# Kernel optimization log

Measured on AMD Instinct MI355X. Metric: run time of the kernel, lower is better.

## Reference

```python
import jax, jax.numpy as jnp
import numpy as np

NF, NA, NC = 100000, 400, 30   # flight, airport, carrier node counts
N = NF + NA + NC               # total nodes after type concatenation
D = 256                        # hidden_channels
B = 3                          # num_bases
R = 4                          # num_relations
E = 250000                     # edges per relation


def setup_inputs() -> dict:
    key = jax.random.key(0)
    ks = jax.random.split(key, 32)
    inp = {
        'x_flight': jax.random.normal(ks[0], (NF, 32), jnp.float32),
        'x_airport': jax.random.normal(ks[1], (NA, 16), jnp.float32),
        'x_carrier': jax.random.normal(ks[2], (NC, 8), jnp.float32),
        # per-type encoders (Linear stored as [in, out])
        'W_f': jax.random.normal(ks[3], (32, D), jnp.float32) * 0.05,
        'b_f': jnp.zeros((D,), jnp.float32),
        'W_a': jax.random.normal(ks[4], (16, D), jnp.float32) * 0.05,
        'b_a': jnp.zeros((D,), jnp.float32),
        'W_c': jax.random.normal(ks[5], (8, D), jnp.float32) * 0.05,
        'b_c': jnp.zeros((D,), jnp.float32),
        # RGCNConv layer 0: basis decomposition W_r = sum_b comp[r,b] * basis[b]
        'basis0': jax.random.normal(ks[6], (B, D, D), jnp.float32) * 0.02,
        'comp0': jax.random.normal(ks[7], (R, B), jnp.float32) * 0.5,
        'root0': jax.random.normal(ks[8], (D, D), jnp.float32) * 0.02,
        'bias0': jnp.zeros((D,), jnp.float32),
        # RGCNConv layer 1
        'basis1': jax.random.normal(ks[9], (B, D, D), jnp.float32) * 0.02,
        'comp1': jax.random.normal(ks[10], (R, B), jnp.float32) * 0.5,
        'root1': jax.random.normal(ks[11], (D, D), jnp.float32) * 0.02,
        'bias1': jnp.zeros((D,), jnp.float32),
        # readout Linear(D -> 1)
        'W_out': jax.random.normal(ks[12], (D, 1), jnp.float32) * 0.05,
        'b_out': jnp.zeros((1,), jnp.float32),
        # per-relation edge lists (local indices within src/dst node type)
        'src0': jax.random.randint(ks[13], (E,), 0, NF),
        'dst0': jax.random.randint(ks[14], (E,), 0, NA),
        'src1': jax.random.randint(ks[15], (E,), 0, NA),
        'dst1': jax.random.randint(ks[16], (E,), 0, NF),
        'src2': jax.random.randint(ks[17], (E,), 0, NF),
        'dst2': jax.random.randint(ks[18], (E,), 0, NC),
        'src3': jax.random.randint(ks[19], (E,), 0, NC),
        'dst3': jax.random.randint(ks[20], (E,), 0, NF),
    }
    return inp


def _rgcn_conv(x, basis, comp, root, bias, edges):
    """PyG RGCNConv with basis decomposition, mean aggregation per relation."""
    W = jnp.einsum('rb,bio->rio', comp, basis)  # [R, D, D]
    out = x @ root + bias                        # root/self transform
    for r, (src, dst) in enumerate(edges):       # R=4 fixed relations
        msg = x[src] @ W[r]                                        # [E, D]
        agg = jax.ops.segment_sum(msg, dst, num_segments=N)        # [N, D]
        deg = jax.ops.segment_sum(jnp.ones((dst.shape[0],), x.dtype), dst,
                                  num_segments=N)
        out = out + agg / jnp.maximum(deg, 1.0)[:, None]           # mean aggr
    return out


def reference(x_flight, x_airport, x_carrier,
              W_f, b_f, W_a, b_a, W_c, b_c,
              basis0, comp0, root0, bias0,
              basis1, comp1, root1, bias1,
              W_out, b_out,
              src0, dst0, src1, dst1, src2, dst2, src3, dst3):
    # per-type encoders + ReLU, then concat into homogeneous node tensor
    hf = jax.nn.relu(x_flight @ W_f + b_f)
    ha = jax.nn.relu(x_airport @ W_a + b_a)
    hc = jax.nn.relu(x_carrier @ W_c + b_c)
    x = jnp.concatenate([hf, ha, hc], axis=0)  # offsets: flight=0, airport=NF, carrier=NF+NA
    edges = [
        (src0, dst0 + NF),        # flight -> airport
        (src1 + NF, dst1),        # airport -> flight
        (src2, dst2 + NF + NA),   # flight -> carrier
        (src3 + NF + NA, dst3),   # carrier -> flight
    ]
    x = jax.nn.relu(_rgcn_conv(x, basis0, comp0, root0, bias0, edges))
    x = jax.nn.relu(_rgcn_conv(x, basis1, comp1, root1, bias1, edges))
    # dropout is identity in eval mode
    return (x[:NF] @ W_out + b_out).squeeze(-1)  # [NF]
```

## Files before the change

### kernel.cpp

```cpp
#include <hip/hip_runtime.h>
#include <hip/hip_bf16.h>
#include <cstdint>
#include <cstddef>

constexpr int NF = 100000;
constexpr int NA = 400;
constexpr int NC = 30;
constexpr int NN = NF + NA + NC;
constexpr int D  = 256;
constexpr int DD = D * D;
constexpr int E  = 250000;
constexpr int NSL = 128;

typedef __attribute__((ext_vector_type(8))) short bf16x8;
typedef __attribute__((ext_vector_type(4))) float f32x4;
typedef __attribute__((ext_vector_type(8))) ushort u16x8;

__device__ inline ushort f2bf(float f) {
    __hip_bfloat16 h = __float2bfloat16(f);
    return __builtin_bit_cast(ushort, h);
}
__device__ inline float bf2f(ushort u) {
    __hip_bfloat16 h = __builtin_bit_cast(__hip_bfloat16, u);
    return __bfloat162float(h);
}

__device__ inline void gload_lds16(const ushort* g, ushort* l) {
    __builtin_amdgcn_global_load_lds(
        (const __attribute__((address_space(1))) void*)g,
        (__attribute__((address_space(3))) void*)l, 16, 0, 0);
}

template<int K, int ROWS>
__global__ __launch_bounds__(256) void encode_kernel(
    const float* __restrict__ x, const float* __restrict__ W,
    const float* __restrict__ b, ushort* __restrict__ hH,
    int rows, int row_off)
{
    int c = threadIdx.x;
    int base = blockIdx.x * ROWS;
    float wcol[K];
    #pragma unroll
    for (int k = 0; k < K; ++k) wcol[k] = W[k * D + c];
    float bias = b[c];
    for (int i = 0; i < ROWS; ++i) {
        int row = base + i;
        if (row >= rows) return;
        const float* xr = x + (size_t)row * K;
        float acc = bias;
        #pragma unroll
        for (int k = 0; k < K; ++k) acc += xr[k] * wcol[k];
        hH[(size_t)(row_off + row) * D + c] = f2bf(fmaxf(acc, 0.f));
    }
}

__global__ __launch_bounds__(256) void wsplit_kernel(
    const float* __restrict__ root, ushort* __restrict__ WtH, ushort* __restrict__ WtL)
{
    int n = blockIdx.x, k = threadIdx.x;
    float w = root[(size_t)k * D + n];
    ushort hi = f2bf(w);
    WtH[(size_t)n * D + k] = hi;
    WtL[(size_t)n * D + k] = f2bf(w - bf2f(hi));
}

__global__ __launch_bounds__(256) void wr_kernel(
    const float* __restrict__ basis, const float* __restrict__ comp,
    float* __restrict__ wr)
{
    int idx = blockIdx.x * 256 + threadIdx.x;
    int r = idx >> 16;
    int io = idx & (DD - 1);
    wr[idx] = comp[r * 3 + 0] * basis[io]
            + comp[r * 3 + 1] * basis[DD + io]
            + comp[r * 3 + 2] * basis[2 * DD + io];
}

__global__ __launch_bounds__(256) void deg_count_kernel(
    const int* __restrict__ dst1, const int* __restrict__ dst3,
    int* __restrict__ deg1, int* __restrict__ deg3)
{
    int idx = blockIdx.x * 256 + threadIdx.x;
    if (idx >= 2 * E) return;
    if (idx < E) atomicAdd(&deg1[dst1[idx]], 1);
    else         atomicAdd(&deg3[dst3[idx - E]], 1);
}

__global__ __launch_bounds__(256) void hist02_kernel(
    const int* __restrict__ dst0, const int* __restrict__ dst2,
    int* __restrict__ bh0, int* __restrict__ bh2)
{
    __shared__ int hist[NA];
    int b = blockIdx.x;
    bool isR2 = (b >= NSL);
    int sl = isR2 ? b - NSL : b;
    const int* dst = isR2 ? dst2 : dst0;
    int nb = isR2 ? NC : NA;
    for (int i = threadIdx.x; i < nb; i += 256) hist[i] = 0;
    __syncthreads();
    int lo = (int)((long long)E * sl / NSL);
    int hi = (int)((long long)E * (sl + 1) / NSL);
    for (int e = lo + threadIdx.x; e < hi; e += 256)
        atomicAdd(&hist[dst[e]], 1);
    __syncthreads();
    int* bh = isR2 ? (bh2 + sl * NC) : (bh0 + sl * NA);
    for (int i = threadIdx.x; i < nb; i += 256) bh[i] = hist[i];
}

__global__ __launch_bounds__(512) void scan02_kernel(
    int* __restrict__ bh0, int* __restrict__ bh2,
    int* __restrict__ rp0, int* __restrict__ rp2,
    float* __restrict__ inv0, float* __restrict__ inv2)
{
    __shared__ int tot[512];
    __shared__ int exc[512];
    int t = threadIdx.x;
    int cnt = 0;
    if (t < NA) {
        int s = 0;
        for (int sl = 0; sl < NSL; ++sl) {
            int v = bh0[sl * NA + t]; bh0[sl * NA + t] = s; s += v;
        }
        cnt = s;
    } else if (t < NA + NC) {
        int bin = t - NA; int s = 0;
        for (int sl = 0; sl < NSL; ++sl) {
            int v = bh2[sl * NC + bin]; bh2[sl * NC + bin] = s; s += v;
        }
        cnt = s;
    }
    tot[t] = cnt;
    __syncthreads();
    for (int ofs = 1; ofs < 512; ofs <<= 1) {
        int v = (t >= ofs) ? tot[t - ofs] : 0;
        __syncthreads();
        tot[t] += v;
        __syncthreads();
    }
    int ex = tot[t] - cnt;
    if (t < NA) {
        exc[t] = ex;
        rp0[t] = ex;
        inv0[t] = 1.0f / (float)(cnt > 1 ? cnt : 1);
        if (t == 0) { rp0[NA] = E; rp2[NC] = E; }
    } else if (t < NA + NC) {
        exc[t] = ex - E;
        rp2[t - NA] = ex - E;
        inv2[t - NA] = 1.0f / (float)(cnt > 1 ? cnt : 1);
    } else exc[t] = 0;
    __syncthreads();
    for (int idx = t; idx < NSL * NA; idx += 512) {
        int sl = idx / NA; int bin = idx - sl * NA;
        bh0[idx] += exc[bin];
    }
    for (int idx = t; idx < NSL * NC; idx += 512) {
        int sl = idx / NC; int bin = idx - sl * NC;
        bh2[idx] += exc[NA + bin];
    }
}

__global__ __launch_bounds__(256) void fill02_kernel(
    const int* __restrict__ src0, const int* __restrict__ dst0,
    const int* __restrict__ src2, const int* __restrict__ dst2,
    const int* __restrict__ bh0, const int* __restrict__ bh2,
    int* __restrict__ csr0, int* __restrict__ csr2)
{
    __shared__ int cur[NA];
    int b = blockIdx.x;
    bool isR2 = (b >= NSL);
    int sl = isR2 ? b - NSL : b;
    const int* src = isR2 ? src2 : src0;
    const int* dst = isR2 ? dst2 : dst0;
    const int* bh  = isR2 ? (bh2 + sl * NC) : (bh0 + sl * NA);
    int* csr       = isR2 ? csr2 : csr0;
    int nb = isR2 ? NC : NA;
    for (int i = threadIdx.x; i < nb; i += 256) cur[i] = bh[i];
    __syncthreads();
    int lo = (int)((long long)E * sl / NSL);
    int hi = (int)((long long)E * (sl + 1) / NSL);
    for (int e = lo + threadIdx.x; e < hi; e += 256) {
        int pos = atomicAdd(&cur[dst[e]], 1);
        csr[pos] = src[e];
    }
}

__global__ __launch_bounds__(1024) void scanA_kernel(
    const int* __restrict__ deg1, const int* __restrict__ deg3, int* __restrict__ bsum)
{
    __shared__ int s[1024];
    int b = blockIdx.x;
    bool isR3 = (b >= 98);
    const int* deg = isR3 ? deg3 : deg1;
    int chunk = isR3 ? b - 98 : b;
    int i = chunk * 1024 + threadIdx.x;
    int v = (i < NF) ? deg[i] : 0;
    s[threadIdx.x] = v;
    __syncthreads();
    for (int ofs = 512; ofs > 0; ofs >>= 1) {
        if ((int)threadIdx.x < ofs) s[threadIdx.x] += s[threadIdx.x + ofs];
        __syncthreads();
    }
    if (threadIdx.x == 0) bsum[(isR3 ? 128 : 0) + chunk] = s[0];
}

__global__ __launch_bounds__(256) void scanB_kernel(int* __restrict__ bsum)
{
    __shared__ int s[256];
    int t = threadIdx.x;
    int v = ((t & 127) < 98) ? bsum[t] : 0;
    s[t] = v;
    __syncthreads();
    for (int ofs = 1; ofs < 128; ofs <<= 1) {
        int a = ((t & 127) >= ofs) ? s[t - ofs] : 0;
        __syncthreads();
        s[t] += a;
        __syncthreads();
    }
    bsum[t] = s[t] - v;
}

__global__ __launch_bounds__(1024) void scanC_kernel(
    const int* __restrict__ deg1, const int* __restrict__ deg3,
    const int* __restrict__ bsum,
    int* __restrict__ rp1, int* __restrict__ rp3,
    int* __restrict__ cu1, int* __restrict__ cu3,
    float* __restrict__ inv1, float* __restrict__ inv3)
{
    __shared__ int s[1024];
    int b = blockIdx.x;
    const int* deg; int* rp; int* cu; float* inv; int chunk; int prefix;
    if (b < 98) { deg = deg1; rp = rp1; cu = cu1; inv = inv1; chunk = b;      prefix = bsum[chunk]; }
    else        { deg = deg3; rp = rp3; cu = cu3; inv = inv3; chunk = b - 98; prefix = bsum[128 + chunk]; }
    int tid = threadIdx.x;
    int i = chunk * 1024 + tid;
    int v = (i < NF) ? deg[i] : 0;
    s[tid] = v;
    __syncthreads();
    for (int ofs = 1; ofs < 1024; ofs <<= 1) {
        int a = (tid >= ofs) ? s[tid - ofs] : 0;
        __syncthreads();
        s[tid] += a;
        __syncthreads();
    }
    int ex = prefix + s[tid] - v;
    if (i < NF) {
        rp[i] = ex;
        cu[i] = ex;
        inv[i] = 1.0f / (float)(v > 1 ? v : 1);
    }
    if (i == 0) rp[NF] = E;
}

__global__ __launch_bounds__(256) void csr_fill13_kernel(
    const int* __restrict__ src1, const int* __restrict__ dst1,
    const int* __restrict__ src3, const int* __restrict__ dst3,
    int* __restrict__ cu1, int* __restrict__ cu3,
    int* __restrict__ csr1, int* __restrict__ csr3)
{
    int idx = blockIdx.x * 256 + threadIdx.x;
    if (idx >= 2 * E) return;
    if (idx < E) {
        int pos = atomicAdd(&cu1[dst1[idx]], 1);
        csr1[pos] = src1[idx];
    } else {
        int e = idx - E;
        int pos = atomicAdd(&cu3[dst3[e]], 1);
        csr3[pos] = src3[e];
    }
}

__global__ __launch_bounds__(256) void y_kernel(
    const ushort* __restrict__ hH, const float* __restrict__ wr,
    float* __restrict__ y)
{
    int row = blockIdx.x;
    int c = threadIdx.x;
    const ushort* sH = hH + (size_t)(NF + row) * D;
    const float* W = wr + (size_t)((row < NA) ? 1 : 3) * DD;
    float acc = 0.f;
    #pragma unroll 8
    for (int k = 0; k < D; ++k) acc += bf2f(sH[k]) * W[k * D + c];
    y[(size_t)row * D + c] = acc;
}

__global__ __launch_bounds__(512) void gemm_mfma(
    const ushort* __restrict__ A,
    const ushort* __restrict__ WtH, const ushort* __restrict__ WtL,
    const float* __restrict__ bias,
    ushort* __restrict__ G, int nrows)
{
    constexpr int BM = 128, BK = 32;
    constexpr int PLANE = BM * BK;
    constexpr int BUF = 3 * PLANE;
    constexpr int LDW = 36;
    __shared__ __align__(16) ushort lds[2 * BUF];
    const int t = threadIdx.x;
    const int row0 = blockIdx.x * BM;
    const int col0 = blockIdx.y * BM;
    const int w = t >> 6, lane = t & 63;
    const int wm = w >> 2, wn = w & 3;
    const int lr = lane & 15;
    const int lk = lane >> 4;
    f32x4 acc[4][2] = {};

    const ushort* sp[3];
    int dofs[3];
    #pragma unroll
    for (int i = 0; i < 3; ++i) {
        int idx = w * 3 + i;
        int plane = idx >> 3, g = idx & 7;
        const ushort* base = (plane == 0) ? A : (plane == 1) ? WtH : WtL;
        int r = ((plane == 0) ? row0 : col0) + g * 16 + lr;
        if (plane == 0 && r >= nrows) r = nrows - 1;
        sp[i] = base + (size_t)r * D + lk * 8;
        dofs[i] = plane * PLANE + g * 512;
    }

    auto stage = [&](int k0, int buf) {
        ushort* bb = lds + buf * BUF;
        #pragma unroll
        for (int i = 0; i < 3; ++i)
            gload_lds16(sp[i] + k0, bb + dofs[i]);
    };
    auto compute = [&](int buf) {
        const ushort* base = lds + buf * BUF;
        const ushort* As  = base;
        const ushort* WsH = base + PLANE;
        const ushort* WsL = base + 2 * PLANE;
        bf16x8 bh[2], bl[2];
        #pragma unroll
        for (int ni = 0; ni < 2; ++ni) {
            int off = (wn * 2 + ni) * 512 + lane * 8;
            bh[ni] = *(const bf16x8*)(&WsH[off]);
            bl[ni] = *(const bf16x8*)(&WsL[off]);
        }
        #pragma unroll
        for (int mi = 0; mi < 4; ++mi) {
            int off = (wm * 4 + mi) * 512 + lane * 8;
            bf16x8 ah = *(const bf16x8*)(&As[off]);
            #pragma unroll
            for (int ni = 0; ni < 2; ++ni) {
                acc[mi][ni] = __builtin_amdgcn_mfma_f32_16x16x32_bf16(ah, bh[ni], acc[mi][ni], 0, 0, 0);
                acc[mi][ni] = __builtin_amdgcn_mfma_f32_16x16x32_bf16(ah, bl[ni], acc[mi][ni], 0, 0, 0);
            }
        }
    };

    stage(0, 0);
    asm volatile("s_waitcnt vmcnt(0)" ::: "memory");
    __builtin_amdgcn_s_barrier();
    __builtin_amdgcn_sched_barrier(0);
    for (int kt = 0; kt < 7; ++kt) {
        stage((kt + 1) * BK, (kt + 1) & 1);
        __builtin_amdgcn_sched_barrier(0);
        compute(kt & 1);
        asm volatile("s_waitcnt vmcnt(0)" ::: "memory");
        __builtin_amdgcn_s_barrier();
        __builtin_amdgcn_sched_barrier(0);
    }
    compute(1);

    __syncthreads();
    float* S = (float*)lds + (size_t)w * 16 * LDW;
    const int rrow = lane >> 2;
    const int grp  = lane & 3;
    #pragma unroll
    for (int mi = 0; mi < 4; ++mi) {
        __syncthreads();
        #pragma unroll
        for (int ni = 0; ni < 2; ++ni)
            #pragma unroll
            for (int reg = 0; reg < 4; ++reg)
                S[(lk * 4 + reg) * LDW + ni * 16 + lr] = acc[mi][ni][reg];
        __syncthreads();
        int gr = row0 + wm * 64 + mi * 16 + rrow;
        int gc = col0 + wn * 32 + grp * 8;
        if (gr >= nrows) continue;
        float4 f0 = *(const float4*)(&S[rrow * LDW + grp * 8]);
        float4 f1 = *(const float4*)(&S[rrow * LDW + grp * 8 + 4]);
        float4 b0 = *(const float4*)(bias + gc);
        float4 b1 = *(const float4*)(bias + gc + 4);
        float v[8] = {f0.x + b0.x, f0.y + b0.y, f0.z + b0.z, f0.w + b0.w,
                      f1.x + b1.x, f1.y + b1.y, f1.z + b1.z, f1.w + b1.w};
        u16x8 hh;
        #pragma unroll
        for (int j = 0; j < 8; ++j) hh[j] = f2bf(v[j]);
        *(u16x8*)(G + (size_t)gr * D + gc) = hh;
    }
}

__global__ __launch_bounds__(256) void msg_relu_kernel(
    ushort* __restrict__ G,
    const float* __restrict__ y,
    const int* __restrict__ rp1, const int* __restrict__ csr1, const float* __restrict__ inv1,
    const int* __restrict__ rp3, const int* __restrict__ csr3, const float* __restrict__ inv3)
{
    int wid = (blockIdx.x * 256 + threadIdx.x) >> 6;
    int lane = threadIdx.x & 63;
    int row = wid * 2 + (lane >> 5);
    if (row >= NF) return;
    int c = (lane & 31) * 8;
    size_t o = (size_t)row * D + c;
    u16x8 gh = *(const u16x8*)(G + o);
    float v[8];
    #pragma unroll
    for (int j = 0; j < 8; ++j) v[j] = bf2f(gh[j]);
    float m[8] = {};
    int e0 = rp1[row], e1 = rp1[row + 1];
    for (int e = e0; e < e1; ++e) {
        const float* yr = y + (size_t)csr1[e] * D + c;
        float4 u0 = *(const float4*)yr;
        float4 u1 = *(const float4*)(yr + 4);
        m[0] += u0.x; m[1] += u0.y; m[2] += u0.z; m[3] += u0.w;
        m[4] += u1.x; m[5] += u1.y; m[6] += u1.z; m[7] += u1.w;
    }
    float s1 = inv1[row];
    #pragma unroll
    for (int j = 0; j < 8; ++j) { v[j] += s1 * m[j]; m[j] = 0.f; }
    e0 = rp3[row]; e1 = rp3[row + 1];
    for (int e = e0; e < e1; ++e) {
        const float* yr = y + (size_t)(NA + csr3[e]) * D + c;
        float4 u0 = *(const float4*)yr;
        float4 u1 = *(const float4*)(yr + 4);
        m[0] += u0.x; m[1] += u0.y; m[2] += u0.z; m[3] += u0.w;
        m[4] += u1.x; m[5] += u1.y; m[6] += u1.z; m[7] += u1.w;
    }
    float s3 = inv3[row];
    u16x8 oh;
    #pragma unroll
    for (int j = 0; j < 8; ++j) oh[j] = f2bf(fmaxf(v[j] + s3 * m[j], 0.f));
    *(u16x8*)(G + o) = oh;
}

__global__ __launch_bounds__(256) void msg_readout_kernel(
    const ushort* __restrict__ G,
    const float* __restrict__ y,
    const int* __restrict__ rp1, const int* __restrict__ csr1, const float* __restrict__ inv1,
    const int* __restrict__ rp3, const int* __restrict__ csr3, const float* __restrict__ inv3,
    const float* __restrict__ wout, const float* __restrict__ bout,
    float* __restrict__ out)
{
    int wid = (blockIdx.x * 256 + threadIdx.x) >> 6;
    int lane = threadIdx.x & 63;
    int row = wid * 2 + (lane >> 5);
    if (row >= NF) return;
    int c = (lane & 31) * 8;
    size_t o = (size_t)row * D + c;
    u16x8 gh = *(const u16x8*)(G + o);
    float v[8];
    #pragma unroll
    for (int j = 0; j < 8; ++j) v[j] = bf2f(gh[j]);
    float m[8] = {};
    int e0 = rp1[row], e1 = rp1[row + 1];
    for (int e = e0; e < e1; ++e) {
        const float* yr = y + (size_t)csr1[e] * D + c;
        float4 u0 = *(const float4*)yr;
        float4 u1 = *(const float4*)(yr + 4);
        m[0] += u0.x; m[1] += u0.y; m[2] += u0.z; m[3] += u0.w;
        m[4] += u1.x; m[5] += u1.y; m[6] += u1.z; m[7] += u1.w;
    }
    float s1 = inv1[row];
    #pragma unroll
    for (int j = 0; j < 8; ++j) { v[j] += s1 * m[j]; m[j] = 0.f; }
    e0 = rp3[row]; e1 = rp3[row + 1];
    for (int e = e0; e < e1; ++e) {
        const float* yr = y + (size_t)(NA + csr3[e]) * D + c;
        float4 u0 = *(const float4*)yr;
        float4 u1 = *(const float4*)(yr + 4);
        m[0] += u0.x; m[1] += u0.y; m[2] += u0.z; m[3] += u0.w;
        m[4] += u1.x; m[5] += u1.y; m[6] += u1.z; m[7] += u1.w;
    }
    float s3 = inv3[row];
    float4 w0 = *(const float4*)(wout + c);
    float4 w1 = *(const float4*)(wout + c + 4);
    float wv[8] = {w0.x, w0.y, w0.z, w0.w, w1.x, w1.y, w1.z, w1.w};
    float pr = 0.f;
    #pragma unroll
    for (int j = 0; j < 8; ++j) pr += fmaxf(v[j] + s3 * m[j], 0.f) * wv[j];
    pr += __shfl_xor(pr, 1);
    pr += __shfl_xor(pr, 2);
    pr += __shfl_xor(pr, 4);
    pr += __shfl_xor(pr, 8);
    pr += __shfl_xor(pr, 16);
    if ((lane & 31) == 0) out[row] = pr + bout[0];
}

__global__ __launch_bounds__(256) void agg_small_kernel(
    const ushort* __restrict__ hH,
    const int* __restrict__ rp0, const int* __restrict__ csr0,
    const int* __restrict__ rp2, const int* __restrict__ csr2,
    float* __restrict__ agg)
{
    __shared__ float red[4][256];
    int b = blockIdx.x;
    const int* rp; const int* csr; int dstn, chunk, nch; float* arow;
    if (b < NA * 4) { dstn = b >> 2; chunk = b & 3; nch = 4;  rp = rp0; csr = csr0; arow = agg + (size_t)dstn * D; }
    else { int bb = b - NA * 4; dstn = bb >> 6; chunk = bb & 63; nch = 64; rp = rp2; csr = csr2; arow = agg + (size_t)(NA + dstn) * D; }
    int s = rp[dstn], e = rp[dstn + 1];
    int cnt = e - s;
    int lo = s + (int)((long long)cnt * chunk / nch);
    int hi = s + (int)((long long)cnt * (chunk + 1) / nch);
    int w = threadIdx.x >> 6, lane = threadIdx.x & 63;
    int span = hi - lo;
    int wlo = lo + (int)((long long)span * w / 4);
    int whi = lo + (int)((long long)span * (w + 1) / 4);
    int half = lane >> 5;
    int ch8 = (lane & 31) * 8;
    float acc[8] = {};
    int p = wlo;
    for (; p + 1 < whi; p += 2) {
        int r = csr[p + half];
        u16x8 v = *(const u16x8*)(hH + (size_t)r * D + ch8);
        #pragma unroll
        for (int j = 0; j < 8; ++j) acc[j] += bf2f(v[j]);
    }
    if (p < whi && half == 0) {
        int r = csr[p];
        u16x8 v = *(const u16x8*)(hH + (size_t)r * D + ch8);
        #pragma unroll
        for (int j = 0; j < 8; ++j) acc[j] += bf2f(v[j]);
    }
    #pragma unroll
    for (int j = 0; j < 8; ++j) acc[j] += __shfl_xor(acc[j], 32);
    if (lane < 32) {
        #pragma unroll
        for (int j = 0; j < 8; ++j) red[w][ch8 + j] = acc[j];
    }
    __syncthreads();
    int c = threadIdx.x;
    float total = red[0][c] + red[1][c] + red[2][c] + red[3][c];
    atomicAdd(arow + c, total);
}

__global__ __launch_bounds__(256) void smallT_kernel(
    const float* __restrict__ agg, const float* __restrict__ wr,
    const float* __restrict__ inv0, const float* __restrict__ inv2,
    ushort* __restrict__ G)
{
    int row = blockIdx.x;
    int c = threadIdx.x;
    const float* a = agg + (size_t)row * D;
    const float* W = wr + (size_t)((row < NA) ? 0 : 2) * DD;
    float scale = (row < NA) ? inv0[row] : inv2[row - NA];
    float acc = 0.f;
    #pragma unroll 8
    for (int k = 0; k < D; ++k) acc += a[k] * W[k * D + c];
    size_t o = (size_t)(NF + row) * D + c;
    G[o] = f2bf(fmaxf(bf2f(G[o]) + scale * acc, 0.f));
}

extern "C" void kernel_launch(void* const* d_in, const int* in_sizes, int n_in,
                              void* d_out, int out_size, void* d_ws, size_t ws_size,
                              hipStream_t stream)
{
    const float* xf = (const float*)d_in[0];
    const float* xa = (const float*)d_in[1];
    const float* xc = (const float*)d_in[2];
    const float* Wf = (const float*)d_in[3];
    const float* bf = (const float*)d_in[4];
    const float* Wa = (const float*)d_in[5];
    const float* ba = (const float*)d_in[6];
    const float* Wc = (const float*)d_in[7];
    const float* bc = (const float*)d_in[8];
    const float* basis0 = (const float*)d_in[9];
    const float* comp0  = (const float*)d_in[10];
    const float* root0  = (const float*)d_in[11];
    const float* bias0  = (const float*)d_in[12];
    const float* basis1 = (const float*)d_in[13];
    const float* comp1  = (const float*)d_in[14];
    const float* root1  = (const float*)d_in[15];
    const float* bias1  = (const float*)d_in[16];
    const float* Wout = (const float*)d_in[17];
    const float* bout = (const float*)d_in[18];
    const int* src0 = (const int*)d_in[19];
    const int* dst0 = (const int*)d_in[20];
    const int* src1 = (const int*)d_in[21];
    const int* dst1 = (const int*)d_in[22];
    const int* src2 = (const int*)d_in[23];
    const int* dst2 = (const int*)d_in[24];
    const int* src3 = (const int*)d_in[25];
    const int* dst3 = (const int*)d_in[26];
    float* out = (float*)d_out;

    char* ws = (char*)d_ws;
    size_t off = 0;
    auto alloc = [&](size_t bytes) -> char* {
        char* p = ws + off;
        off = (off + bytes + 255) & ~(size_t)255;
        return p;
    };
    ushort* hH  = (ushort*)alloc((size_t)NN * D * 2);
    ushort* gH  = (ushort*)alloc((size_t)NN * D * 2);
    ushort* g2H = hH;
    ushort* WtH = (ushort*)alloc((size_t)DD * 2);
    ushort* WtL = (ushort*)alloc((size_t)DD * 2);
    float* wrbuf  = (float*)alloc((size_t)4 * DD * 4);
    float* ybuf   = (float*)alloc((size_t)(NA + NC) * D * 4);
    float* aggbuf = (float*)alloc((size_t)(NA + NC) * D * 4);
    int*   deg13  = (int*)  alloc((size_t)2 * NF * 4);
    int* deg1 = deg13; int* deg3 = deg13 + NF;
    float* inv1 = (float*)alloc((size_t)NF * 4);
    float* inv3 = (float*)alloc((size_t)NF * 4);
    float* inv0 = (float*)alloc((size_t)NA * 4);
    float* inv2 = (float*)alloc((size_t)NC * 4);
    int* rp0 = (int*)alloc((NA + 1) * 4);
    int* rp1 = (int*)alloc((size_t)(NF + 1) * 4);
    int* rp2 = (int*)alloc((NC + 1) * 4);
    int* rp3 = (int*)alloc((size_t)(NF + 1) * 4);
    int* cu1 = (int*)alloc((size_t)(NF + 1) * 4);
    int* cu3 = (int*)alloc((size_t)(NF + 1) * 4);
    int* csr0 = (int*)alloc((size_t)E * 4);
    int* csr1 = (int*)alloc((size_t)E * 4);
    int* csr2 = (int*)alloc((size_t)E * 4);
    int* csr3 = (int*)alloc((size_t)E * 4);
    int* bsum = (int*)alloc(256 * 4);
    int* bh0  = (int*)alloc((size_t)NSL * NA * 4);
    int* bh2  = (int*)alloc((size_t)NSL * NC * 4);
    (void)ws_size; (void)in_sizes; (void)n_in; (void)out_size;

    hist02_kernel<<<2 * NSL, 256, 0, stream>>>(dst0, dst2, bh0, bh2);
    scan02_kernel<<<1, 512, 0, stream>>>(bh0, bh2, rp0, rp2, inv0, inv2);
    fill02_kernel<<<2 * NSL, 256, 0, stream>>>(src0, dst0, src2, dst2, bh0, bh2, csr0, csr2);

    hipMemsetAsync(deg13, 0, (size_t)2 * NF * 4, stream);
    deg_count_kernel<<<(2 * E + 255) / 256, 256, 0, stream>>>(dst1, dst3, deg1, deg3);
    scanA_kernel<<<196, 1024, 0, stream>>>(deg1, deg3, bsum);
    scanB_kernel<<<1, 256, 0, stream>>>(bsum);
    scanC_kernel<<<196, 1024, 0, stream>>>(deg1, deg3, bsum, rp1, rp3, cu1, cu3, inv1, inv3);
    csr_fill13_kernel<<<(2 * E + 255) / 256, 256, 0, stream>>>(
        src1, dst1, src3, dst3, cu1, cu3, csr1, csr3);

    encode_kernel<32, 8><<<NF / 8, 256, 0, stream>>>(xf, Wf, bf, hH, NF, 0);
    encode_kernel<16, 8><<<(NA + 7) / 8, 256, 0, stream>>>(xa, Wa, ba, hH, NA, NF);
    encode_kernel<8, 8><<<(NC + 7) / 8, 256, 0, stream>>>(xc, Wc, bc, hH, NC, NF + NA);

    wsplit_kernel<<<D, D, 0, stream>>>(root0, WtH, WtL);
    wr_kernel<<<4 * DD / 256, 256, 0, stream>>>(basis0, comp0, wrbuf);
    y_kernel<<<NA + NC, 256, 0, stream>>>(hH, wrbuf, ybuf);
    gemm_mfma<<<dim3((NN + 127) / 128, 2), 512, 0, stream>>>(
        hH, WtH, WtL, bias0, gH, NN);
    hipMemsetAsync(aggbuf, 0, (size_t)(NA + NC) * D * 4, stream);
    agg_small_kernel<<<NA * 4 + NC * 64, 256, 0, stream>>>(
        hH, rp0, csr0, rp2, csr2, aggbuf);
    smallT_kernel<<<NA + NC, 256, 0, stream>>>(aggbuf, wrbuf, inv0, inv2, gH);
    msg_relu_kernel<<<(NF / 2 * 64 + 255) / 256, 256, 0, stream>>>(
        gH, ybuf, rp1, csr1, inv1, rp3, csr3, inv3);

    wsplit_kernel<<<D, D, 0, stream>>>(root1, WtH, WtL);
    wr_kernel<<<4 * DD / 256, 256, 0, stream>>>(basis1, comp1, wrbuf);
    y_kernel<<<NA + NC, 256, 0, stream>>>(gH, wrbuf, ybuf);
    gemm_mfma<<<dim3((NF + 127) / 128, 2), 512, 0, stream>>>(
        gH, WtH, WtL, bias1, g2H, NF);
    msg_readout_kernel<<<(NF / 2 * 64 + 255) / 256, 256, 0, stream>>>(
        g2H, ybuf, rp1, csr1, inv1, rp3, csr3, inv3, Wout, bout, out);
}
```

Baseline: 402.9 us.

## Triple-buffer GEMM K-loop and widen per-lane columns in message kernels

The MFMA GEMM moves from a double-buffered to a triple-buffered LDS pipeline. It keeps two tiles of global-to-LDS loads in flight and waits on partial vmcnt counts instead of draining all loads every step. Separately, the message-passing and readout kernels now handle 16 columns per lane and 4 rows per wavefront instead of 8 columns and 2 rows, so each thread issues more independent loads per gathered edge. This adds LDS footprint, which may lower GEMM occupancy, and raises register pressure in the gather kernels.

```diff
diff --git a/kernel.cpp b/kernel.cpp
--- a/kernel.cpp
+++ b/kernel.cpp
@@ -293,7 +293,7 @@
     constexpr int PLANE = BM * BK;
     constexpr int BUF = 3 * PLANE;
     constexpr int LDW = 36;
-    __shared__ __align__(16) ushort lds[2 * BUF];
+    __shared__ __align__(16) ushort lds[3 * BUF];
     const int t = threadIdx.x;
     const int row0 = blockIdx.x * BM;
     const int col0 = blockIdx.y * BM;
@@ -316,8 +316,9 @@
         dofs[i] = plane * PLANE + g * 512;
     }
 
-    auto stage = [&](int k0, int buf) {
+    auto stage = [&](int kt, int buf) {
         ushort* bb = lds + buf * BUF;
+        int k0 = kt * BK;
         #pragma unroll
         for (int i = 0; i < 3; ++i)
             gload_lds16(sp[i] + k0, bb + dofs[i]);
@@ -347,18 +348,25 @@
     };
 
     stage(0, 0);
-    asm volatile("s_waitcnt vmcnt(0)" ::: "memory");
-    __builtin_amdgcn_s_barrier();
-    __builtin_amdgcn_sched_barrier(0);
-    for (int kt = 0; kt < 7; ++kt) {
-        stage((kt + 1) * BK, (kt + 1) & 1);
-        __builtin_amdgcn_sched_barrier(0);
-        compute(kt & 1);
-        asm volatile("s_waitcnt vmcnt(0)" ::: "memory");
-        __builtin_amdgcn_s_barrier();
-        __builtin_amdgcn_sched_barrier(0);
-    }
-    compute(1);
+    stage(1, 1);
+    stage(2, 2);
+#define PIPE_ITER(KT, PEND)                                        \
+    asm volatile("s_waitcnt vmcnt(" #PEND ")" ::: "memory");       \
+    __builtin_amdgcn_s_barrier();                                  \
+    __builtin_amdgcn_sched_barrier(0);                             \
+    compute((KT) % 3);                                             \
+    __builtin_amdgcn_s_barrier();                                  \
+    __builtin_amdgcn_sched_barrier(0);                             \
+    if ((KT) + 3 < 8) stage((KT) + 3, (KT) % 3);
+    PIPE_ITER(0, 6)
+    PIPE_ITER(1, 6)
+    PIPE_ITER(2, 6)
+    PIPE_ITER(3, 6)
+    PIPE_ITER(4, 6)
+    PIPE_ITER(5, 6)
+    PIPE_ITER(6, 3)
+    PIPE_ITER(7, 0)
+#undef PIPE_ITER
 
     __syncthreads();
     float* S = (float*)lds + (size_t)w * 16 * LDW;
@@ -397,39 +405,48 @@
 {
     int wid = (blockIdx.x * 256 + threadIdx.x) >> 6;
     int lane = threadIdx.x & 63;
-    int row = wid * 2 + (lane >> 5);
+    int row = wid * 4 + (lane >> 4);
     if (row >= NF) return;
-    int c = (lane & 31) * 8;
+    int c = (lane & 15) * 16;
     size_t o = (size_t)row * D + c;
-    u16x8 gh = *(const u16x8*)(G + o);
-    float v[8];
-    #pragma unroll
-    for (int j = 0; j < 8; ++j) v[j] = bf2f(gh[j]);
-    float m[8] = {};
+    u16x8 g0 = *(const u16x8*)(G + o);
+    u16x8 g1 = *(const u16x8*)(G + o + 8);
+    float v[16];
+    #pragma unroll
+    for (int j = 0; j < 8; ++j) { v[j] = bf2f(g0[j]); v[8 + j] = bf2f(g1[j]); }
+    float m[16] = {};
     int e0 = rp1[row], e1 = rp1[row + 1];
     for (int e = e0; e < e1; ++e) {
         const float* yr = y + (size_t)csr1[e] * D + c;
-        float4 u0 = *(const float4*)yr;
-        float4 u1 = *(const float4*)(yr + 4);
-        m[0] += u0.x; m[1] += u0.y; m[2] += u0.z; m[3] += u0.w;
-        m[4] += u1.x; m[5] += u1.y; m[6] += u1.z; m[7] += u1.w;
+        #pragma unroll
+        for (int q = 0; q < 4; ++q) {
+            float4 u = *(const float4*)(yr + q * 4);
+            m[q * 4 + 0] += u.x; m[q * 4 + 1] += u.y;
+            m[q * 4 + 2] += u.z; m[q * 4 + 3] += u.w;
+        }
     }
     float s1 = inv1[row];
     #pragma unroll
-    for (int j = 0; j < 8; ++j) { v[j] += s1 * m[j]; m[j] = 0.f; }
+    for (int j = 0; j < 16; ++j) { v[j] += s1 * m[j]; m[j] = 0.f; }
     e0 = rp3[row]; e1 = rp3[row + 1];
     for (int e = e0; e < e1; ++e) {
         const float* yr = y + (size_t)(NA + csr3[e]) * D + c;
-        float4 u0 = *(const float4*)yr;
-        float4 u1 = *(const float4*)(yr + 4);
-        m[0] += u0.x; m[1] += u0.y; m[2] += u0.z; m[3] += u0.w;
-        m[4] += u1.x; m[5] += u1.y; m[6] += u1.z; m[7] += u1.w;
+        #pragma unroll
+        for (int q = 0; q < 4; ++q) {
+            float4 u = *(const float4*)(yr + q * 4);
+            m[q * 4 + 0] += u.x; m[q * 4 + 1] += u.y;
+            m[q * 4 + 2] += u.z; m[q * 4 + 3] += u.w;
+        }
     }
     float s3 = inv3[row];
-    u16x8 oh;
-    #pragma unroll
-    for (int j = 0; j < 8; ++j) oh[j] = f2bf(fmaxf(v[j] + s3 * m[j], 0.f));
-    *(u16x8*)(G + o) = oh;
+    u16x8 o0, o1;
+    #pragma unroll
+    for (int j = 0; j < 8; ++j) {
+        o0[j] = f2bf(fmaxf(v[j] + s3 * m[j], 0.f));
+        o1[j] = f2bf(fmaxf(v[8 + j] + s3 * m[8 + j], 0.f));
+    }
+    *(u16x8*)(G + o) = o0;
+    *(u16x8*)(G + o + 8) = o1;
 }
 
 __global__ __launch_bounds__(256) void msg_readout_kernel(
@@ -442,47 +459,54 @@
 {
     int wid = (blockIdx.x * 256 + threadIdx.x) >> 6;
     int lane = threadIdx.x & 63;
-    int row = wid * 2 + (lane >> 5);
+    int row = wid * 4 + (lane >> 4);
     if (row >= NF) return;
-    int c = (lane & 31) * 8;
+    int c = (lane & 15) * 16;
     size_t o = (size_t)row * D + c;
-    u16x8 gh = *(const u16x8*)(G + o);
-    float v[8];
-    #pragma unroll
-    for (int j = 0; j < 8; ++j) v[j] = bf2f(gh[j]);
-    float m[8] = {};
+    u16x8 g0 = *(const u16x8*)(G + o);
+    u16x8 g1 = *(const u16x8*)(G + o + 8);
+    float v[16];
+    #pragma unroll
+    for (int j = 0; j < 8; ++j) { v[j] = bf2f(g0[j]); v[8 + j] = bf2f(g1[j]); }
+    float m[16] = {};
     int e0 = rp1[row], e1 = rp1[row + 1];
     for (int e = e0; e < e1; ++e) {
         const float* yr = y + (size_t)csr1[e] * D + c;
-        float4 u0 = *(const float4*)yr;
-        float4 u1 = *(const float4*)(yr + 4);
-        m[0] += u0.x; m[1] += u0.y; m[2] += u0.z; m[3] += u0.w;
-        m[4] += u1.x; m[5] += u1.y; m[6] += u1.z; m[7] += u1.w;
+        #pragma unroll
+        for (int q = 0; q < 4; ++q) {
+            float4 u = *(const float4*)(yr + q * 4);
+            m[q * 4 + 0] += u.x; m[q * 4 + 1] += u.y;
+            m[q * 4 + 2] += u.z; m[q * 4 + 3] += u.w;
+        }
     }
     float s1 = inv1[row];
     #pragma unroll
-    for (int j = 0; j < 8; ++j) { v[j] += s1 * m[j]; m[j] = 0.f; }
+    for (int j = 0; j < 16; ++j) { v[j] += s1 * m[j]; m[j] = 0.f; }
     e0 = rp3[row]; e1 = rp3[row + 1];
     for (int e = e0; e < e1; ++e) {
         const float* yr = y + (size_t)(NA + csr3[e]) * D + c;
-        float4 u0 = *(const float4*)yr;
-        float4 u1 = *(const float4*)(yr + 4);
-        m[0] += u0.x; m[1] += u0.y; m[2] += u0.z; m[3] += u0.w;
-        m[4] += u1.x; m[5] += u1.y; m[6] += u1.z; m[7] += u1.w;
+        #pragma unroll
+        for (int q = 0; q < 4; ++q) {
+            float4 u = *(const float4*)(yr + q * 4);
+            m[q * 4 + 0] += u.x; m[q * 4 + 1] += u.y;
+            m[q * 4 + 2] += u.z; m[q * 4 + 3] += u.w;
+        }
     }
     float s3 = inv3[row];
-    float4 w0 = *(const float4*)(wout + c);
-    float4 w1 = *(const float4*)(wout + c + 4);
-    float wv[8] = {w0.x, w0.y, w0.z, w0.w, w1.x, w1.y, w1.z, w1.w};
     float pr = 0.f;
     #pragma unroll
-    for (int j = 0; j < 8; ++j) pr += fmaxf(v[j] + s3 * m[j], 0.f) * wv[j];
+    for (int q = 0; q < 4; ++q) {
+        float4 wq = *(const float4*)(wout + c + q * 4);
+        pr += fmaxf(v[q*4+0] + s3 * m[q*4+0], 0.f) * wq.x
+            + fmaxf(v[q*4+1] + s3 * m[q*4+1], 0.f) * wq.y
+            + fmaxf(v[q*4+2] + s3 * m[q*4+2], 0.f) * wq.z
+            + fmaxf(v[q*4+3] + s3 * m[q*4+3], 0.f) * wq.w;
+    }
     pr += __shfl_xor(pr, 1);
     pr += __shfl_xor(pr, 2);
     pr += __shfl_xor(pr, 4);
     pr += __shfl_xor(pr, 8);
-    pr += __shfl_xor(pr, 16);
-    if ((lane & 31) == 0) out[row] = pr + bout[0];
+    if ((lane & 15) == 0) out[row] = pr + bout[0];
 }
 
 __global__ __launch_bounds__(256) void agg_small_kernel(
@@ -643,7 +667,7 @@
     agg_small_kernel<<<NA * 4 + NC * 64, 256, 0, stream>>>(
         hH, rp0, csr0, rp2, csr2, aggbuf);
     smallT_kernel<<<NA + NC, 256, 0, stream>>>(aggbuf, wrbuf, inv0, inv2, gH);
-    msg_relu_kernel<<<(NF / 2 * 64 + 255) / 256, 256, 0, stream>>>(
+    msg_relu_kernel<<<(NF / 4 * 64 + 255) / 256, 256, 0, stream>>>(
         gH, ybuf, rp1, csr1, inv1, rp3, csr3, inv3);
 
     wsplit_kernel<<<D, D, 0, stream>>>(root1, WtH, WtL);
@@ -651,6 +675,6 @@
     y_kernel<<<NA + NC, 256, 0, stream>>>(gH, wrbuf, ybuf);
     gemm_mfma<<<dim3((NF + 127) / 128, 2), 512, 0, stream>>>(
         gH, WtH, WtL, bias1, g2H, NF);
-    msg_readout_kernel<<<(NF / 2 * 64 + 255) / 256, 256, 0, stream>>>(
+    msg_readout_kernel<<<(NF / 4 * 64 + 255) / 256, 256, 0, stream>>>(
         g2H, ybuf, rp1, csr1, inv1, rp3, csr3, inv3, Wout, bout, out);
 }
```

Result: slower. 419.4 us (+4.1%).
